# Performance work log

Hardware: AMD Instinct MI355X
Metric: run time of the kernel (lower is better)

## Reference

```python
import jax, jax.numpy as jnp
import numpy as np

EMBED = 1024
HEADS = 16
B, T = 2, 2048


def setup_inputs() -> dict:
    key = jax.random.key(0)
    k1, k2, k3, k4, k5 = jax.random.split(key, 5)
    C = EMBED
    x = jax.random.normal(k1, (B, T, C), dtype=jnp.float32)
    # torch Linear(C, 3C): weight [3C, C]; store transposed for x @ W
    W_kqv = jax.random.normal(k2, (C, 3 * C), dtype=jnp.float32) * (1.0 / np.sqrt(C))
    b_kqv = jax.random.normal(k3, (3 * C,), dtype=jnp.float32) * 0.02
    W_out = jax.random.normal(k4, (C, C), dtype=jnp.float32) * (1.0 / np.sqrt(C))
    b_out = jax.random.normal(k5, (C,), dtype=jnp.float32) * 0.02
    return {"x": x, "W_kqv": W_kqv, "b_kqv": b_kqv, "W_out": W_out, "b_out": b_out}


def reference(x, W_kqv, b_kqv, W_out, b_out):
    Bsz, Tlen, C = x.shape
    H = HEADS
    Dh = C // H
    qkv = x @ W_kqv + b_kqv                       # [B, T, 3C]
    q, k, v = jnp.split(qkv, 3, axis=-1)
    # [B, H, T, Dh]
    q = q.reshape(Bsz, Tlen, H, Dh).transpose(0, 2, 1, 3)
    k = k.reshape(Bsz, Tlen, H, Dh).transpose(0, 2, 1, 3)
    v = v.reshape(Bsz, Tlen, H, Dh).transpose(0, 2, 1, 3)
    att = jnp.einsum('bhqd,bhkd->bhqk', q, k) * (1.0 / np.sqrt(Dh))
    causal = jnp.triu(jnp.ones((Tlen, Tlen), dtype=bool), k=1)  # True above diag
    att = jnp.where(causal[None, None, :, :], -jnp.inf, att)
    att = jax.nn.softmax(att, axis=-1)
    y = jnp.einsum('bhqk,bhkd->bhqd', att, v)     # [B, H, T, Dh]
    y = y.transpose(0, 2, 1, 3).reshape(Bsz, Tlen, C)
    return y @ W_out + b_out
```

## Files before the change

### kernel.cpp

```cpp
#include <hip/hip_runtime.h>
#include <math.h>

#define EMBED 1024
#define NH    16
#define DH    64
#define BATCH 2
#define SEQ   2048
#define MTOT  4096
#define BHTOT 32

typedef float f32x4  __attribute__((ext_vector_type(4)));
typedef float f32x16 __attribute__((ext_vector_type(16)));
typedef short s16x8  __attribute__((ext_vector_type(8)));
typedef short s16x4  __attribute__((ext_vector_type(4)));
typedef unsigned u32x2 __attribute__((ext_vector_type(2)));
typedef unsigned u32x4 __attribute__((ext_vector_type(4)));

#define AS1 __attribute__((address_space(1)))
#define AS3 __attribute__((address_space(3)))

__device__ __forceinline__ unsigned short bf16_rne(float f) {
    unsigned u = __builtin_bit_cast(unsigned, f);
    return (unsigned short)((u + 0x7FFFu + ((u >> 16) & 1u)) >> 16);
}
__device__ __forceinline__ void gload16(const void* g, void* l) {
    __builtin_amdgcn_global_load_lds((const AS1 void*)g, (AS3 void*)l, 16, 0, 0);
}
__device__ __forceinline__ unsigned cvt_pk_bf16(float lo, float hi) {
    unsigned r;
    asm volatile("v_cvt_pk_bf16_f32 %0, %1, %2" : "=v"(r) : "v"(lo), "v"(hi));
    return r;
}
#define EXP2(x) __builtin_amdgcn_exp2f(x)
#define MFMA16(a, b, c) __builtin_amdgcn_mfma_f32_16x16x32_bf16((a), (b), (c), 0, 0, 0)
#define MFMA32(a, b, c) __builtin_amdgcn_mfma_f32_32x32x16_bf16((a), (b), (c), 0, 0, 0)

__global__ __launch_bounds__(256)
void prep_kernel(const float* __restrict__ X, const float* __restrict__ Wkqv,
                 const float* __restrict__ Wout,
                 unsigned short* __restrict__ Xh,
                 unsigned short* __restrict__ WhT,
                 unsigned short* __restrict__ WoTh)
{
    __shared__ float T[32][33];
    const int bid = blockIdx.x, tid = threadIdx.x;

    if (bid < 2048) {
        const size_t i = ((size_t)bid * 256 + tid) * 8;
        float4 a = *(const float4*)&X[i];
        float4 b = *(const float4*)&X[i + 4];
        float v[8] = {a.x, a.y, a.z, a.w, b.x, b.y, b.z, b.w};
        s16x8 h8;
#pragma unroll
        for (int e = 0; e < 8; ++e) h8[e] = (short)bf16_rne(v[e]);
        *(s16x8*)&Xh[i] = h8;
        return;
    }

    const float* W;
    unsigned short* Hi;
    int Nd, n0, k0;
    if (bid < 5120) {
        const int u = bid - 2048;
        W = Wkqv; Hi = WhT; Nd = 3072;
        n0 = (u % 96) * 32; k0 = (u / 96) * 32;
    } else {
        const int u = bid - 5120;
        W = Wout; Hi = WoTh; Nd = 1024;
        n0 = (u & 31) * 32; k0 = (u >> 5) * 32;
    }
    constexpr int Kd = 1024;
    {
        const int row = tid >> 3, c4 = (tid & 7) * 4;
        float4 v = *(const float4*)&W[(size_t)(k0 + row) * Nd + n0 + c4];
        T[row][c4] = v.x; T[row][c4 + 1] = v.y; T[row][c4 + 2] = v.z; T[row][c4 + 3] = v.w;
    }
    __syncthreads();
    {
        const int nr = tid >> 3, c4 = (tid & 7) * 4;
        s16x4 h4;
#pragma unroll
        for (int e = 0; e < 4; ++e) h4[e] = (short)bf16_rne(T[c4 + e][nr]);
        *(s16x4*)&Hi[(size_t)(n0 + nr) * Kd + k0 + c4] = h4;
    }
}

__global__ __launch_bounds__(256)
void qkv_gemm_kernel(const unsigned short* __restrict__ Xh_g,
                     const unsigned short* __restrict__ BhT,
                     const float* __restrict__ bias,
                     unsigned short* __restrict__ Qh,
                     unsigned short* __restrict__ Kh,
                     unsigned short* __restrict__ Vh)
{
    constexpr int KD = 1024;
    __shared__ __align__(16) short SB[2][8192];

    const int tid = threadIdx.x, lane = tid & 63, wid = tid >> 6;
    const int l31 = lane & 31, l5 = lane >> 5;
    const int wm = wid >> 1, wn = wid & 1;

    const int bid = blockIdx.x;
    const int u = bid >> 3, xcd = bid & 7;
    const int by = xcd * 4 + (u & 3);
    const int bx = u >> 2;
    const int m0 = by * 128, n0 = bx * 128;

    f32x16 acc[2][2];
#pragma unroll
    for (int i = 0; i < 2; ++i)
#pragma unroll
        for (int j = 0; j < 2; ++j)
#pragma unroll
            for (int e = 0; e < 16; ++e) acc[i][j][e] = 0.f;

    const int srow = lane >> 2, ss = lane & 3;

    {
#pragma unroll
        for (int i = 0; i < 4; ++i) {
            const int s = wid * 4 + i;
            const int t = s >> 3, j = s & 7;
            const unsigned short* gsrc = (t == 0) ? Xh_g : BhT;
            const int roff = (t == 0) ? m0 : n0;
            const int row_loc = j * 16 + srow;
            const int kc = ss ^ ((row_loc >> 1) & 3);
            gload16(gsrc + (size_t)(roff + row_loc) * KD + kc * 8,
                    &SB[0][t * 4096 + j * 512]);
        }
    }

    for (int it = 0; it < 32; ++it) {
        const int cur = it & 1;
        __syncthreads();
        if (it + 1 < 32) {
            const int k0n = (it + 1) * 32;
#pragma unroll
            for (int i = 0; i < 4; ++i) {
                const int s = wid * 4 + i;
                const int t = s >> 3, j = s & 7;
                const unsigned short* gsrc = (t == 0) ? Xh_g : BhT;
                const int roff = (t == 0) ? m0 : n0;
                const int row_loc = j * 16 + srow;
                const int kc = ss ^ ((row_loc >> 1) & 3);
                gload16(gsrc + (size_t)(roff + row_loc) * KD + k0n + kc * 8,
                        &SB[cur ^ 1][t * 4096 + j * 512]);
            }
        }
        const short* Ahp = &SB[cur][0];
        const short* Bhp = &SB[cur][4096];

        s16x8 fa[2][2], fbh[2][2];
#pragma unroll
        for (int am = 0; am < 2; ++am) {
            const int row = wm * 64 + am * 32 + l31;
            const int sw = (row >> 1) & 3;
#pragma unroll
            for (int kh2 = 0; kh2 < 2; ++kh2) {
                const int sl = ((kh2 * 2 + l5) ^ sw) * 8;
                fa[am][kh2] = *(const s16x8*)&Ahp[row * 32 + sl];
            }
        }
#pragma unroll
        for (int bn = 0; bn < 2; ++bn) {
            const int row = wn * 64 + bn * 32 + l31;
            const int sw = (row >> 1) & 3;
#pragma unroll
            for (int kh2 = 0; kh2 < 2; ++kh2) {
                const int sl = ((kh2 * 2 + l5) ^ sw) * 8;
                fbh[bn][kh2] = *(const s16x8*)&Bhp[row * 32 + sl];
            }
        }
#pragma unroll
        for (int kh2 = 0; kh2 < 2; ++kh2)
#pragma unroll
            for (int am = 0; am < 2; ++am)
#pragma unroll
                for (int bn = 0; bn < 2; ++bn)
                    acc[am][bn] = MFMA32(fa[am][kh2], fbh[bn][kh2], acc[am][bn]);
    }

    const float QSCALE = 0.125f * 1.44269504f;
#pragma unroll
    for (int am = 0; am < 2; ++am)
#pragma unroll
        for (int bn = 0; bn < 2; ++bn) {
            const int n = n0 + wn * 64 + bn * 32 + l31;
            const float bv = bias[n];
            const int sec = n >> 10, cc = n & 1023, h = cc >> 6, d = cc & 63;
#pragma unroll
            for (int r = 0; r < 16; ++r) {
                const int mrow = (r & 3) + 8 * (r >> 2) + 4 * l5;
                const int m = m0 + wm * 64 + am * 32 + mrow;
                const int bb = m >> 11, t = m & 2047;
                const int bh_i = bb * NH + h;
                float val = acc[am][bn][r] + bv;
                if (sec == 0) {
                    size_t idx = ((size_t)bh_i * SEQ + t) * DH + d;
                    Qh[idx] = bf16_rne(val * QSCALE);
                } else if (sec == 1) {
                    size_t idx = ((size_t)bh_i * SEQ + t) * DH + d;
                    Kh[idx] = bf16_rne(val);
                } else {
                    size_t idx = ((size_t)bh_i * DH + d) * SEQ + t;
                    Vh[idx] = bf16_rne(val);
                }
            }
        }
}

__global__ __launch_bounds__(256)
void attn_kernel(const unsigned short* __restrict__ Qh_g,
                 const unsigned short* __restrict__ Kh_g,
                 const unsigned short* __restrict__ Vh_g,
                 unsigned short* __restrict__ Yh)
{
    __shared__ __align__(16) short SM[2][8192];

    const int tid = threadIdx.x, lane = tid & 63, wid = tid >> 6;
    const int l31 = lane & 31, l5 = lane >> 5;
    const int bid = blockIdx.x;
    const int qb = 15 - (bid >> 5), bh = bid & 31;
    const int Q0 = qb * 128;
    const int qg = Q0 + wid * 32 + l31;

    s16x8 qfh[4];
    {
        const size_t qo = ((size_t)bh * SEQ + qg) * DH;
#pragma unroll
        for (int t = 0; t < 4; ++t) {
            const int ch = t * 2 + l5;
            qfh[t] = *(const s16x8*)&Qh_g[qo + ch * 8];
        }
    }

    float m_i = -INFINITY, l_i = 0.f;
    f32x16 yacc[2];
#pragma unroll
    for (int e = 0; e < 16; ++e) { yacc[0][e] = 0.f; yacc[1][e] = 0.f; }

    const int srow = lane >> 3, ss = lane & 7;
    const int KT = 2 * qb + 2;

    {
#pragma unroll
        for (int i = 0; i < 4; ++i) {
            const int s = wid * 4 + i;
            const int t = s >> 3, j = s & 7;
            const int row = j * 8 + srow;
            const int kc = ss ^ (row & 7);
            const unsigned short* src = (t == 0)
                ? Kh_g + ((size_t)bh * SEQ + row) * DH + kc * 8
                : Vh_g + ((size_t)bh * DH + row) * SEQ + kc * 8;
            gload16(src, &SM[0][t * 4096 + j * 512]);
        }
    }

    for (int kt = 0; kt < KT; ++kt) {
        const int cur = kt & 1;
        __syncthreads();
        if (kt + 1 < KT) {
            const int kn = (kt + 1) * 64;
#pragma unroll
            for (int i = 0; i < 4; ++i) {
                const int s = wid * 4 + i;
                const int t = s >> 3, j = s & 7;
                const int row = j * 8 + srow;
                const int kc = ss ^ (row & 7);
                const unsigned short* src = (t == 0)
                    ? Kh_g + ((size_t)bh * SEQ + kn + row) * DH + kc * 8
                    : Vh_g + ((size_t)bh * DH + row) * SEQ + kn + kc * 8;
                gload16(src, &SM[cur ^ 1][t * 4096 + j * 512]);
            }
        }

        if (kt * 64 > Q0 + wid * 32 + 31) continue;

        const short* Ksh = &SM[cur][0];
        const short* Vsh = &SM[cur][4096];

        f32x16 s[2];
#pragma unroll
        for (int e = 0; e < 16; ++e) { s[0][e] = 0.f; s[1][e] = 0.f; }
#pragma unroll
        for (int t = 0; t < 4; ++t) {
            s16x8 kh[2];
#pragma unroll
            for (int kb = 0; kb < 2; ++kb) {
                const int row = kb * 32 + l31;
                const int sl = ((t * 2 + l5) ^ (row & 7)) * 8;
                kh[kb] = *(const s16x8*)&Ksh[row * 64 + sl];
            }
#pragma unroll
            for (int kb = 0; kb < 2; ++kb) s[kb] = MFMA32(kh[kb], qfh[t], s[kb]);
        }

        if (kt * 64 + 63 > Q0 + wid * 32) {
#pragma unroll
            for (int kb = 0; kb < 2; ++kb)
#pragma unroll
                for (int r = 0; r < 16; ++r) {
                    const int key = kt * 64 + kb * 32 + (r & 3) + 8 * (r >> 2) + 4 * l5;
                    if (key > qg) s[kb][r] = -INFINITY;
                }
        }

        float mx = s[0][0];
#pragma unroll
        for (int r = 1; r < 16; ++r) mx = fmaxf(mx, s[0][r]);
#pragma unroll
        for (int r = 0; r < 16; ++r) mx = fmaxf(mx, s[1][r]);
        mx = fmaxf(mx, __shfl_xor(mx, 32));
        const bool defer = (__all(mx - m_i <= 8.f) != 0);
        float mref;
        if (defer) {
            mref = m_i;
        } else {
            mref = fmaxf(m_i, mx);
            const float al = EXP2(m_i - mref);
            m_i = mref;
            l_i *= al;
#pragma unroll
            for (int e = 0; e < 16; ++e) { yacc[0][e] *= al; yacc[1][e] *= al; }
        }
        float ls = 0.f;
#pragma unroll
        for (int kb = 0; kb < 2; ++kb)
#pragma unroll
            for (int r = 0; r < 16; ++r) {
                s[kb][r] = EXP2(s[kb][r] - mref);
                ls += s[kb][r];
            }
        ls += __shfl_xor(ls, 32);
        l_i += ls;

        unsigned pk[2][8];
#pragma unroll
        for (int kb = 0; kb < 2; ++kb)
#pragma unroll
            for (int j = 0; j < 8; ++j)
                pk[kb][j] = cvt_pk_bf16(s[kb][2 * j], s[kb][2 * j + 1]);
        s16x8 pf[2][2];
#pragma unroll
        for (int kb = 0; kb < 2; ++kb) {
            u32x2 sA = __builtin_amdgcn_permlane32_swap(pk[kb][0], pk[kb][2], false, false);
            u32x2 sB = __builtin_amdgcn_permlane32_swap(pk[kb][1], pk[kb][3], false, false);
            u32x4 w0 = {sA[0], sB[0], sA[1], sB[1]};
            pf[kb][0] = __builtin_bit_cast(s16x8, w0);
            u32x2 sC = __builtin_amdgcn_permlane32_swap(pk[kb][4], pk[kb][6], false, false);
            u32x2 sD = __builtin_amdgcn_permlane32_swap(pk[kb][5], pk[kb][7], false, false);
            u32x4 w1 = {sC[0], sD[0], sC[1], sD[1]};
            pf[kb][1] = __builtin_bit_cast(s16x8, w1);
        }

#pragma unroll
        for (int t = 0; t < 4; ++t) {
            s16x8 vh[2];
#pragma unroll
            for (int dt = 0; dt < 2; ++dt) {
                const int row = dt * 32 + l31;
                const int sl = ((t * 2 + l5) ^ (row & 7)) * 8;
                vh[dt] = *(const s16x8*)&Vsh[row * 64 + sl];
            }
            const s16x8 pfr = pf[t >> 1][t & 1];
#pragma unroll
            for (int dt = 0; dt < 2; ++dt) yacc[dt] = MFMA32(vh[dt], pfr, yacc[dt]);
        }
    }

    __syncthreads();
    short* SMf = &SM[0][0];
    const float inv = 1.f / l_i;
    const int qlcl = wid * 32 + l31;
#pragma unroll
    for (int dt = 0; dt < 2; ++dt)
#pragma unroll
        for (int rq = 0; rq < 4; ++rq) {
            const int d0 = dt * 32 + rq * 8 + 4 * l5;
            s16x4 h4;
#pragma unroll
            for (int c = 0; c < 4; ++c)
                h4[c] = (short)bf16_rne(yacc[dt][rq * 4 + c] * inv);
            const int base = qlcl * 64 + (((d0 >> 3) ^ (qlcl & 7)) * 8) + (d0 & 7);
            *(s16x4*)&SMf[base] = h4;
        }
    __syncthreads();
    const int b = bh >> 4, h = bh & 15;
#pragma unroll
    for (int i = 0; i < 4; ++i) {
        const int idx = tid + i * 256;
        const int row = idx >> 3, ch = idx & 7;
        const int sl = (ch ^ (row & 7)) * 8;
        s16x8 vh8 = *(const s16x8*)&SMf[row * 64 + sl];
        const size_t o = ((size_t)(b * SEQ + Q0 + row)) * EMBED + h * DH + ch * 8;
        *(s16x8*)&Yh[o] = vh8;
    }
}

__global__ __launch_bounds__(256)
void out_gemm_kernel(const unsigned short* __restrict__ Yh_g,
                     const unsigned short* __restrict__ WhT,
                     const float* __restrict__ bias, float* __restrict__ out)
{
    constexpr int KD = 1024, ND = 1024;
    __shared__ __align__(16) short SB[2][6144];

    const int tid = threadIdx.x, lane = tid & 63, wid = tid >> 6;
    const int g = lane >> 4, ln = lane & 15;
    const int wm = wid >> 1, wn = wid & 1;

    const int bid = blockIdx.x;
    const int u = bid >> 3, xcd = bid & 7;
    const int by = xcd * 4 + (u & 3);
    const int bx = u >> 2;
    const int m0 = by * 128, n0 = bx * 64;

    f32x4 acc[4][2];
#pragma unroll
    for (int i = 0; i < 4; ++i)
#pragma unroll
        for (int j = 0; j < 2; ++j) acc[i][j] = (f32x4){0.f, 0.f, 0.f, 0.f};

    const int srow = lane >> 2, ss = lane & 3;

#define OG_STAGE(buf, k0_)                                                     \
    {                                                                          \
        _Pragma("unroll")                                                      \
        for (int i = 0; i < 3; ++i) {                                          \
            const int s = wid * 3 + i;                                         \
            const bool isA = (s < 8);                                          \
            const int j = isA ? s : (s - 8);                                   \
            const int row_loc = j * 16 + srow;                                 \
            const int kc = ss ^ ((row_loc >> 1) & 3);                          \
            const unsigned short* src = isA                                    \
                ? Yh_g + (size_t)(m0 + row_loc) * KD + (k0_) + kc * 8          \
                : WhT + (size_t)(n0 + row_loc) * KD + (k0_) + kc * 8;          \
            gload16(src, &SB[buf][(isA ? 0 : 4096) + j * 512]);                \
        }                                                                      \
    }

    OG_STAGE(0, 0)

    for (int it = 0; it < 32; ++it) {
        const int cur = it & 1;
        __syncthreads();
        if (it + 1 < 32) OG_STAGE(cur ^ 1, (it + 1) * 32)

        const short* Ah = &SB[cur][0];
        const short* Bh = &SB[cur][4096];

        s16x8 fah[4], fbh[2];
#pragma unroll
        for (int am = 0; am < 4; ++am) {
            int m_loc = wm * 64 + am * 16 + ln;
            int sl = (g ^ ((m_loc >> 1) & 3)) * 8;
            fah[am] = *(const s16x8*)&Ah[m_loc * 32 + sl];
        }
#pragma unroll
        for (int bn = 0; bn < 2; ++bn) {
            int n_loc = wn * 32 + bn * 16 + ln;
            int sl = (g ^ ((n_loc >> 1) & 3)) * 8;
            fbh[bn] = *(const s16x8*)&Bh[n_loc * 32 + sl];
        }
#pragma unroll
        for (int am = 0; am < 4; ++am)
#pragma unroll
            for (int bn = 0; bn < 2; ++bn)
                acc[am][bn] = MFMA16(fah[am], fbh[bn], acc[am][bn]);
    }
#undef OG_STAGE

#pragma unroll
    for (int am = 0; am < 4; ++am)
#pragma unroll
        for (int bn = 0; bn < 2; ++bn) {
            int n = n0 + wn * 32 + bn * 16 + ln;
            float bv = bias[n];
#pragma unroll
            for (int r = 0; r < 4; ++r) {
                int m = m0 + wm * 64 + am * 16 + g * 4 + r;
                out[(size_t)m * ND + n] = acc[am][bn][r] + bv;
            }
        }
}

extern "C" void kernel_launch(void* const* d_in, const int* in_sizes, int n_in,
                              void* d_out, int out_size, void* d_ws, size_t ws_size,
                              hipStream_t stream)
{
    const float* x     = (const float*)d_in[0];
    const float* W_kqv = (const float*)d_in[1];
    const float* b_kqv = (const float*)d_in[2];
    const float* W_out = (const float*)d_in[3];
    const float* b_out = (const float*)d_in[4];
    float* out = (float*)d_out;

    char* ws = (char*)d_ws;
    const size_t MB = 1024 * 1024;
    unsigned short* Qh   = (unsigned short*)(ws);
    unsigned short* WoTh = (unsigned short*)(ws + 8 * MB);
    unsigned short* Kh   = Qh + 8388608;
    unsigned short* Vh   = Kh + 8388608;
    unsigned short* WhT  = (unsigned short*)(ws + 48 * MB);
    unsigned short* Yh   = (unsigned short*)(ws + 48 * MB);
    unsigned short* Xh = (unsigned short*)d_out;

    prep_kernel<<<dim3(6144), 256, 0, stream>>>(
        x, W_kqv, W_out, Xh, WhT, WoTh);
    qkv_gemm_kernel<<<dim3(768), 256, 0, stream>>>(
        Xh, WhT, b_kqv, Qh, Kh, Vh);
    attn_kernel<<<dim3(BHTOT * (SEQ / 128)), 256, 0, stream>>>(
        Qh, Kh, Vh, Yh);
    out_gemm_kernel<<<dim3(512), 256, 0, stream>>>(
        Yh, WoTh, b_out, out);
}
```

Measured before the change: 114.7 us.

## Triple-buffer QKV GEMM shared-memory loads with explicit vmcnt waits

Moves the QKV projection GEMM main loop from double to triple buffering of LDS tiles, issuing global-to-LDS loads two iterations ahead. Explicit s_waitcnt vmcnt counts and raw s_barrier calls replace __syncthreads so outstanding loads can stay in flight across iterations. This is meant to hide global load latency behind MFMA work. The cost is 50% more LDS per block, which may lower occupancy, and correctness now depends on the hand-set waitcnt values matching the number of loads issued.

```diff
diff --git a/kernel.cpp b/kernel.cpp
--- a/kernel.cpp
+++ b/kernel.cpp
@@ -94,7 +94,7 @@
                      unsigned short* __restrict__ Vh)
 {
     constexpr int KD = 1024;
-    __shared__ __align__(16) short SB[2][8192];
+    __shared__ __align__(16) short SB[3][8192];
 
     const int tid = threadIdx.x, lane = tid & 63, wid = tid >> 6;
     const int l31 = lane & 31, l5 = lane >> 5;
@@ -116,37 +116,37 @@
 
     const int srow = lane >> 2, ss = lane & 3;
 
-    {
-#pragma unroll
-        for (int i = 0; i < 4; ++i) {
-            const int s = wid * 4 + i;
-            const int t = s >> 3, j = s & 7;
-            const unsigned short* gsrc = (t == 0) ? Xh_g : BhT;
-            const int roff = (t == 0) ? m0 : n0;
-            const int row_loc = j * 16 + srow;
-            const int kc = ss ^ ((row_loc >> 1) & 3);
-            gload16(gsrc + (size_t)(roff + row_loc) * KD + kc * 8,
-                    &SB[0][t * 4096 + j * 512]);
-        }
-    }
+#define QK_STAGE(buf, k0_)                                                     \
+    {                                                                          \
+        _Pragma("unroll")                                                      \
+        for (int i = 0; i < 4; ++i) {                                          \
+            const int s = wid * 4 + i;                                         \
+            const int t = s >> 3, j = s & 7;                                   \
+            const unsigned short* gsrc = (t == 0) ? Xh_g : BhT;                \
+            const int roff = (t == 0) ? m0 : n0;                               \
+            const int row_loc = j * 16 + srow;                                 \
+            const int kc = ss ^ ((row_loc >> 1) & 3);                          \
+            gload16(gsrc + (size_t)(roff + row_loc) * KD + (k0_) + kc * 8,     \
+                    &SB[buf][t * 4096 + j * 512]);                             \
+        }                                                                      \
+    }
+
+    QK_STAGE(0, 0)
+    QK_STAGE(1, 32)
 
     for (int it = 0; it < 32; ++it) {
-        const int cur = it & 1;
-        __syncthreads();
-        if (it + 1 < 32) {
-            const int k0n = (it + 1) * 32;
-#pragma unroll
-            for (int i = 0; i < 4; ++i) {
-                const int s = wid * 4 + i;
-                const int t = s >> 3, j = s & 7;
-                const unsigned short* gsrc = (t == 0) ? Xh_g : BhT;
-                const int roff = (t == 0) ? m0 : n0;
-                const int row_loc = j * 16 + srow;
-                const int kc = ss ^ ((row_loc >> 1) & 3);
-                gload16(gsrc + (size_t)(roff + row_loc) * KD + k0n + kc * 8,
-                        &SB[cur ^ 1][t * 4096 + j * 512]);
-            }
-        }
+        const int cur = it % 3;
+        if (it + 2 < 32) {
+            QK_STAGE((it + 2) % 3, (it + 2) * 32)
+            asm volatile("s_waitcnt vmcnt(8)" ::: "memory");
+        } else if (it + 1 < 32) {
+            asm volatile("s_waitcnt vmcnt(4)" ::: "memory");
+        } else {
+            asm volatile("s_waitcnt vmcnt(0)" ::: "memory");
+        }
+        __builtin_amdgcn_s_barrier();
+        __builtin_amdgcn_sched_barrier(0);
+
         const short* Ahp = &SB[cur][0];
         const short* Bhp = &SB[cur][4096];
 
@@ -178,7 +178,10 @@
 #pragma unroll
                 for (int bn = 0; bn < 2; ++bn)
                     acc[am][bn] = MFMA32(fa[am][kh2], fbh[bn][kh2], acc[am][bn]);
-    }
+
+        __builtin_amdgcn_s_barrier();
+    }
+#undef QK_STAGE
 
     const float QSCALE = 0.125f * 1.44269504f;
 #pragma unroll
```

Result: no change. 115.6 us (+0.8%).
